# Kernel optimization log

Measured on AMD Instinct MI355X. Metric: run time of the kernel, lower is better.

The kernel has to match this reference:

```python
import jax, jax.numpy as jnp
import numpy as np
import math

B, S, D, H = 2, 2048, 1024, 16
DK = D // H

def setup_inputs() -> dict:
    key = jax.random.key(0)
    ks = jax.random.split(key, 12)
    s = 1.0 / math.sqrt(D)
    inp = {
        'input_q': jax.random.normal(ks[0], (B, S, D), jnp.float32),
        'input_k': jax.random.normal(ks[1], (B, S, D), jnp.float32),
        'input_v': jax.random.normal(ks[2], (B, S, D), jnp.float32),
        'mask': jax.random.randint(ks[3], (B, 1, S, S), 0, 2, jnp.int32),
        'Wq': jax.random.normal(ks[4], (D, D), jnp.float32) * s,
        'bq': jnp.zeros((D,), jnp.float32),
        'Wk': jax.random.normal(ks[5], (D, D), jnp.float32) * s,
        'bk': jnp.zeros((D,), jnp.float32),
        'Wv': jax.random.normal(ks[6], (D, D), jnp.float32) * s,
        'bv': jnp.zeros((D,), jnp.float32),
        'Wo': jax.random.normal(ks[7], (D, D), jnp.float32) * s,
        'bo': jnp.zeros((D,), jnp.float32),
    }
    return inp

def reference(input_q, input_k, input_v, mask, Wq, bq, Wk, bk, Wv, bv, Wo, bo):
    # Linear projections (torch Linear: x @ W.T + b), split into heads: [B,H,S,DK]
    q = (input_q @ Wq.T + bq).reshape(B, S, H, DK).transpose(0, 2, 1, 3)
    k = (input_k @ Wk.T + bk).reshape(B, S, H, DK).transpose(0, 2, 1, 3)
    v = (input_v @ Wv.T + bv).reshape(B, S, H, DK).transpose(0, 2, 1, 3)
    scores = jnp.einsum('bhqd,bhkd->bhqk', q, k) / math.sqrt(DK)
    scores = jnp.where(mask == 0, jnp.float32(-1e9), scores)
    attn = jax.nn.softmax(scores, axis=-1)
    out = jnp.einsum('bhqk,bhkd->bhqd', attn, v)
    out = out.transpose(0, 2, 1, 3).reshape(B, S, D)
    return out @ Wo.T + bo
```

## Files before the change

### kernel.cpp

```cpp
#include <hip/hip_runtime.h>
#include <math.h>

#define kB 2
#define kS 2048
#define kD 1024
#define kH 16
#define kM (kB * kS)

#define kC 0.180336880f

typedef unsigned short u16;
typedef unsigned int u32;
typedef unsigned long long u64;
typedef short s16x8 __attribute__((ext_vector_type(8)));
typedef float f32x4 __attribute__((ext_vector_type(4)));

__device__ __forceinline__ u16 f2bf(float f) {
    u32 u = __float_as_uint(f);
    u += 0x7FFFu + ((u >> 16) & 1u);
    return (u16)(u >> 16);
}

__device__ __forceinline__ u32 cvt_pk_bf16(float lo, float hi) {
    u32 r;
    asm("v_cvt_pk_bf16_f32 %0, %1, %2" : "=v"(r) : "v"(lo), "v"(hi));
    return r;
}

typedef __attribute__((address_space(1))) void as1_void;
typedef __attribute__((address_space(3))) void as3_void;
__device__ __forceinline__ void async_copy16(const void* g, void* l) {
    __builtin_amdgcn_global_load_lds((as1_void*)(unsigned long long)g,
                                     (as3_void*)(unsigned)(unsigned long long)l,
                                     16, 0, 0);
}

__global__ __launch_bounds__(256) void prep(
        const float* __restrict__ xq, const float* __restrict__ xk, const float* __restrict__ xv,
        const float* __restrict__ Wq, const float* __restrict__ Wk,
        const float* __restrict__ Wv, const float* __restrict__ Wo,
        const int* __restrict__ msk,
        u16* __restrict__ xqb, u16* __restrict__ xkb, u16* __restrict__ xvb,
        u16* __restrict__ wqb, u16* __restrict__ wkb, u16* __restrict__ wvb,
        u16* __restrict__ wob, u64* __restrict__ prepM) {
    const int bid = blockIdx.x;
    const int tid = threadIdx.x;
    if (bid < 16384) {
        const float* in;
        u16* out;
        int i;
        float sc = 1.0f;
        if (bid < 12288) {
            const int z = bid >> 12;
            in = z == 0 ? xq : (z == 1 ? xk : xv);
            out = z == 0 ? xqb : (z == 1 ? xkb : xvb);
            i = (bid & 4095) * 256 + tid;
        } else {
            const int z = (bid - 12288) >> 10;
            in = z == 0 ? Wq : (z == 1 ? Wk : (z == 2 ? Wv : Wo));
            out = z == 0 ? wqb : (z == 1 ? wkb : (z == 2 ? wvb : wob));
            if (z == 0) sc = kC;
            i = ((bid - 12288) & 1023) * 256 + tid;
        }
        const float4 v = ((const float4*)in)[i];
        ushort4 o;
        o.x = f2bf(v.x * sc); o.y = f2bf(v.y * sc);
        o.z = f2bf(v.z * sc); o.w = f2bf(v.w * sc);
        ((ushort4*)out)[i] = o;
    } else {
        const int wid = (bid - 16384) * 4 + (tid >> 6);
        const int lane = tid & 63;
        const int kt = wid & 31, qb = (wid >> 5) & 127, b = wid >> 12;
        const int q = qb * 16 + (lane & 15);
        const int kbase = kt * 64 + ((lane >> 4) << 2);
        const int* mrow = msk + ((size_t)b * kS + q) * kS;
        u64 keep = 0;
#pragma unroll
        for (int e = 0; e < 16; ++e) {
            const int k = kbase + (e >> 2) * 16 + (e & 3);
            const u64 bl = __ballot(mrow[k] != 0);
            if (lane == e) keep = bl;
        }
        if (lane < 16)
            prepM[(((size_t)b * 128 + qb) * 32 + kt) * 16 + lane] = keep;
    }
}

template <int MODE, int TILEM>
__device__ __forceinline__ void gemm_bt_body(const u16* __restrict__ A,
                                             const u16* __restrict__ W,
                                             const float* __restrict__ bias,
                                             void* __restrict__ Cp,
                                             const float bscale) {
    constexpr int FM = TILEM / 32;
    __shared__ u16 As[TILEM * 64];
    __shared__ u16 Bs[128 * 64];
    const int tid = threadIdx.x;
    const int wave = tid >> 6, lane = tid & 63;
    const int l15 = lane & 15, quad = lane >> 4, l7 = lane & 7;
    const int wr = wave >> 1, wc = wave & 1;
    const int m0 = (MODE == 3 ? blockIdx.x : blockIdx.y) * TILEM;
    const int n0 = (MODE == 3 ? blockIdx.y : blockIdx.x) * 128;

    const int srow = lane >> 3;
    const int schk = l7 ^ srow;
    const u16* gA = A + (size_t)(m0 + (TILEM / 4) * wave + srow) * kD + schk * 8;
    const u16* gB = W + (size_t)(n0 + 32 * wave + srow) * kD + schk * 8;
    u16* lA = As + ((TILEM / 4) * wave) * 64;
    u16* lB = Bs + (32 * wave) * 64;

    f32x4 acc[FM][4];
#pragma unroll
    for (int i = 0; i < FM; ++i)
#pragma unroll
        for (int j = 0; j < 4; ++j) acc[i][j] = (f32x4)0.f;

    for (int kt = 0; kt < kD; kt += 64) {
        __syncthreads();
#pragma unroll
        for (int i = 0; i < TILEM / 32; ++i)
            async_copy16(gA + (size_t)(8 * i) * kD + kt, lA + (8 * i) * 64);
#pragma unroll
        for (int i = 0; i < 4; ++i)
            async_copy16(gB + (size_t)(8 * i) * kD + kt, lB + (8 * i) * 64);
        __syncthreads();

#pragma unroll
        for (int s = 0; s < 2; ++s) {
            const int rdoff = ((s * 4 + quad) ^ l7) * 8;
            s16x8 af[FM], bf[4];
#pragma unroll
            for (int fm = 0; fm < FM; ++fm)
                af[fm] = *(const s16x8*)(As + (wr * (TILEM / 2) + fm * 16 + l15) * 64 + rdoff);
#pragma unroll
            for (int fn = 0; fn < 4; ++fn)
                bf[fn] = *(const s16x8*)(Bs + (wc * 64 + fn * 16 + l15) * 64 + rdoff);
#pragma unroll
            for (int fm = 0; fm < FM; ++fm)
#pragma unroll
                for (int fn = 0; fn < 4; ++fn)
                    acc[fm][fn] = __builtin_amdgcn_mfma_f32_16x16x32_bf16(
                        af[fm], bf[fn], acc[fm][fn], 0, 0, 0);
        }
    }

    if constexpr (MODE == 3) {
#pragma unroll
        for (int fn = 0; fn < 4; ++fn) {
            const int sglob = n0 + wc * 64 + fn * 16 + l15;
            const int bb = sglob >> 11, ss = sglob & (kS - 1);
#pragma unroll
            for (int fm = 0; fm < FM; ++fm) {
                const int dglob = m0 + wr * (TILEM / 2) + fm * 16 + quad * 4;
                const float4 b4 = *(const float4*)(bias + dglob);
                const float bb4[4] = {b4.x * bscale, b4.y * bscale,
                                      b4.z * bscale, b4.w * bscale};
                const int hh = dglob >> 6, dd = dglob & 63;
                u16* base = (u16*)Cp + ((size_t)(bb * kH + hh) * 64 + dd) * kS + ss;
#pragma unroll
                for (int r = 0; r < 4; ++r)
                    base[(size_t)r * kS] = f2bf(acc[fm][fn][r] + bb4[r]);
            }
        }
    } else {
#pragma unroll
        for (int fn = 0; fn < 4; ++fn) {
            const int col = n0 + wc * 64 + fn * 16 + l15;
            const float bv = bias[col] * bscale;
#pragma unroll
            for (int fm = 0; fm < FM; ++fm) {
                const int row = m0 + wr * (TILEM / 2) + fm * 16 + quad * 4;
#pragma unroll
                for (int r = 0; r < 4; ++r) {
                    const float v = acc[fm][fn][r] + bv;
                    if constexpr (MODE == 0)
                        ((u16*)Cp)[(size_t)(row + r) * kD + col] = f2bf(v);
                    else
                        ((float*)Cp)[(size_t)(row + r) * kD + col] = v;
                }
            }
        }
    }
}

__global__ __launch_bounds__(256) void qkv_gemm(
        const u16* __restrict__ xq, const u16* __restrict__ xk, const u16* __restrict__ xv,
        const u16* __restrict__ wq, const u16* __restrict__ wk, const u16* __restrict__ wv,
        const float* __restrict__ bq, const float* __restrict__ bk, const float* __restrict__ bv,
        u16* __restrict__ q, u16* __restrict__ k, u16* __restrict__ vt) {
    const int z = blockIdx.z;
    if (z == 0)      gemm_bt_body<0, 128>(xq, wq, bq, q, kC);
    else if (z == 1) gemm_bt_body<0, 128>(xk, wk, bk, k, 1.f);
    else             gemm_bt_body<3, 128>(wv, xv, bv, vt, 1.f);
}

__global__ __launch_bounds__(256) void o_gemm(const u16* __restrict__ A,
                                              const u16* __restrict__ W,
                                              const float* __restrict__ bias,
                                              float* __restrict__ C) {
    gemm_bt_body<2, 64>(A, W, bias, C, 1.f);
}

__global__ __launch_bounds__(256) void attn_mfma(const u16* __restrict__ Qb,
                                                 const u16* __restrict__ Kb,
                                                 const u16* __restrict__ Vt,
                                                 const u64* __restrict__ prepM,
                                                 u16* __restrict__ Ob) {
    __shared__ u16 Qs[64 * 64];
    __shared__ u16 Ks[64 * 64];
    __shared__ u16 Vs[64 * 64];
    __shared__ u16 Ps[64 * 64];

    const int tid = threadIdx.x;
    const int wave = tid >> 6, lane = tid & 63;
    const int l15 = lane & 15, quad = lane >> 4, l7 = lane & 7;
    const int q0 = blockIdx.x * 64;
    const int b = blockIdx.y >> 4, h = blockIdx.y & 15;

    const int srow = lane >> 3;
    const int schk = l7 ^ srow;

    {
        const u16* g0 = Qb + ((size_t)(b * kS + q0 + 16 * wave + srow)) * kD + h * 64 + schk * 8;
        async_copy16(g0, Qs + (16 * wave) * 64);
        async_copy16(g0 + 8 * kD, Qs + (16 * wave + 8) * 64);
    }
    const u16* gK0 = Kb + ((size_t)(b * kS + 16 * wave + srow)) * kD + h * 64 + schk * 8;
    const u16* gV0 = Vt + ((size_t)((b * kH + h) * 64 + 16 * wave + srow)) * kS + schk * 8;

    const int wave_u = __builtin_amdgcn_readfirstlane(wave);
    const u64* mbase = prepM + (((size_t)b * 128 + blockIdx.x * 4 + wave_u) * 32) * 16;

    s16x8 onesf;
#pragma unroll
    for (int i = 0; i < 8; ++i) onesf[i] = (short)0x3F80;

    f32x4 oacc[4];
#pragma unroll
    for (int i = 0; i < 4; ++i) oacc[i] = (f32x4)0.f;
    f32x4 lacc = (f32x4)0.f;

    __syncthreads();
    s16x8 bq[2];
    bq[0] = *(const s16x8*)(Qs + (16 * wave + l15) * 64 + ((0 + quad) ^ l7) * 8);
    bq[1] = *(const s16x8*)(Qs + (16 * wave + l15) * 64 + ((4 + quad) ^ l7) * 8);
    u16* psrow = Ps + (16 * wave + l15) * 64;

    for (int kt = 0; kt < kS; kt += 64) {
        __syncthreads();
        async_copy16(gK0 + (size_t)kt * kD, Ks + (16 * wave) * 64);
        async_copy16(gK0 + (size_t)(kt + 8) * kD, Ks + (16 * wave + 8) * 64);
        async_copy16(gV0 + kt, Vs + (16 * wave) * 64);
        async_copy16(gV0 + 8 * kS + kt, Vs + (16 * wave + 8) * 64);
        __syncthreads();

        f32x4 s[4];
#pragma unroll
        for (int fn = 0; fn < 4; ++fn) s[fn] = (f32x4)0.f;
#pragma unroll
        for (int kc = 0; kc < 2; ++kc)
#pragma unroll
            for (int fn = 0; fn < 4; ++fn) {
                const s16x8 ak = *(const s16x8*)(Ks + (fn * 16 + l15) * 64 + ((kc * 4 + quad) ^ l7) * 8);
                s[fn] = __builtin_amdgcn_mfma_f32_16x16x32_bf16(ak, bq[kc], s[fn], 0, 0, 0);
            }

        const u64* mt = mbase + (kt >> 6) * 16;
#pragma unroll
        for (int fn = 0; fn < 4; ++fn)
#pragma unroll
            for (int r = 0; r < 4; ++r) {
                const u64 mm = mt[fn * 4 + r];
                const float p = exp2f(s[fn][r]);
                float pm;
                asm("v_cndmask_b32 %0, 0, %1, %2" : "=v"(pm) : "v"(p), "s"(mm));
                s[fn][r] = pm;
            }

#pragma unroll
        for (int fn = 0; fn < 4; ++fn) {
            uint2 o;
            o.x = cvt_pk_bf16(s[fn][0], s[fn][1]);
            o.y = cvt_pk_bf16(s[fn][2], s[fn][3]);
            const int chunk = fn * 2 + (quad >> 1);
            *(uint2*)(psrow + ((chunk ^ l7) * 8) + (quad & 1) * 4) = o;
        }

#pragma unroll
        for (int kc = 0; kc < 2; ++kc) {
            const s16x8 bp = *(const s16x8*)(psrow + ((kc * 4 + quad) ^ l7) * 8);
            lacc = __builtin_amdgcn_mfma_f32_16x16x32_bf16(onesf, bp, lacc, 0, 0, 0);
#pragma unroll
            for (int fd = 0; fd < 4; ++fd) {
                const s16x8 av = *(const s16x8*)(Vs + (fd * 16 + l15) * 64 + ((kc * 4 + quad) ^ l7) * 8);
                oacc[fd] = __builtin_amdgcn_mfma_f32_16x16x32_bf16(av, bp, oacc[fd], 0, 0, 0);
            }
        }
    }

    const float inv = 1.f / lacc[0];
    const size_t orow = (size_t)(b * kS + q0 + 16 * wave + l15);
#pragma unroll
    for (int fd = 0; fd < 4; ++fd) {
        uint2 o;
        o.x = cvt_pk_bf16(oacc[fd][0] * inv, oacc[fd][1] * inv);
        o.y = cvt_pk_bf16(oacc[fd][2] * inv, oacc[fd][3] * inv);
        *(uint2*)(Ob + orow * kD + h * 64 + fd * 16 + quad * 4) = o;
    }
}

extern "C" void kernel_launch(void* const* d_in, const int* in_sizes, int n_in,
                              void* d_out, int out_size, void* d_ws, size_t ws_size,
                              hipStream_t stream) {
    const float* xq = (const float*)d_in[0];
    const float* xk = (const float*)d_in[1];
    const float* xv = (const float*)d_in[2];
    const int*  msk = (const int*)d_in[3];
    const float* Wq = (const float*)d_in[4];
    const float* bq = (const float*)d_in[5];
    const float* Wk = (const float*)d_in[6];
    const float* bk = (const float*)d_in[7];
    const float* Wv = (const float*)d_in[8];
    const float* bv = (const float*)d_in[9];
    const float* Wo = (const float*)d_in[10];
    const float* bo = (const float*)d_in[11];
    float* out = (float*)d_out;

    const size_t NX = (size_t)kM * kD;
    const size_t NW = (size_t)kD * kD;

    u64* prepM = (u64*)d_ws;
    u16* p = (u16*)((char*)d_ws + (1 << 20));
    u16* xqb = p; p += NX;
    u16* xkb = p; p += NX;
    u16* xvb = p; p += NX;
    u16* wqb = p; p += NW;
    u16* wkb = p; p += NW;
    u16* wvb = p; p += NW;
    u16* wob = p; p += NW;
    u16* qb  = p; p += NX;
    u16* kb  = p; p += NX;
    u16* vtb = p; p += NX;
    u16* ab  = xqb;

    prep<<<18432, 256, 0, stream>>>(xq, xk, xv, Wq, Wk, Wv, Wo, msk,
                                    xqb, xkb, xvb, wqb, wkb, wvb, wob, prepM);

    dim3 gq(kD / 128, kM / 128, 3);
    qkv_gemm<<<gq, 256, 0, stream>>>(xqb, xkb, xvb, wqb, wkb, wvb, bq, bk, bv, qb, kb, vtb);

    dim3 ga(kS / 64, kB * kH);
    attn_mfma<<<ga, 256, 0, stream>>>(qb, kb, vtb, prepM, ab);

    dim3 go(kD / 128, kM / 64);
    o_gemm<<<go, 256, 0, stream>>>(ab, wob, bo, out);
}
```

Measured before the change: 274.1 us.

## Double-buffer K/V tiles in attention with prefetch and MFMA priority hints

Restructures the attention loop so the next K/V tile is copied asynchronously into a second LDS buffer while the current tile is computed. This replaces the two barriers per iteration with one, and hides global load latency behind the MFMA work. It also preloads the mask words and V fragments into registers early, uses the hardware exp2 builtin, and raises wave priority around the MFMA sections. Q is staged in the P buffer to save LDS. The cost is higher LDS and register use, which may reduce occupancy.

```diff
diff --git a/kernel.cpp b/kernel.cpp
--- a/kernel.cpp
+++ b/kernel.cpp
@@ -14,6 +14,12 @@
 typedef unsigned long long u64;
 typedef short s16x8 __attribute__((ext_vector_type(8)));
 typedef float f32x4 __attribute__((ext_vector_type(4)));
+
+#if __has_builtin(__builtin_amdgcn_exp2f)
+#define EXP2(x) __builtin_amdgcn_exp2f(x)
+#else
+#define EXP2(x) exp2f(x)
+#endif
 
 __device__ __forceinline__ u16 f2bf(float f) {
     u32 u = __float_as_uint(f);
@@ -201,15 +207,86 @@
     gemm_bt_body<2, 64>(A, W, bias, C, 1.f);
 }
 
+__device__ __forceinline__ void attn_tile(
+        const int kt, u16* __restrict__ cur, u16* __restrict__ nxt, const bool do_stage,
+        const u16* __restrict__ gK0, const u16* __restrict__ gV0,
+        const u64* __restrict__ mbase,
+        const s16x8 bq0, const s16x8 bq1, const s16x8 onesf,
+        u16* __restrict__ psrow,
+        f32x4 oacc[4], f32x4& lacc,
+        const int l15, const int quad, const int l7, const int wave) {
+    if (do_stage) {
+        async_copy16(gK0 + (size_t)(kt + 64) * kD, nxt + (16 * wave) * 64);
+        async_copy16(gK0 + (size_t)(kt + 72) * kD, nxt + (16 * wave + 8) * 64);
+        async_copy16(gV0 + kt + 64, nxt + 4096 + (16 * wave) * 64);
+        async_copy16(gV0 + 8 * kS + kt + 64, nxt + 4096 + (16 * wave + 8) * 64);
+    }
+    const u64* mt = mbase + (kt >> 6) * 16;
+    u64 mk[16];
+#pragma unroll
+    for (int i = 0; i < 16; ++i) mk[i] = mt[i];
+
+    f32x4 s[4];
+#pragma unroll
+    for (int fn = 0; fn < 4; ++fn) s[fn] = (f32x4)0.f;
+    __builtin_amdgcn_s_setprio(1);
+#pragma unroll
+    for (int kc = 0; kc < 2; ++kc) {
+        const s16x8 bqf = kc ? bq1 : bq0;
+#pragma unroll
+        for (int fn = 0; fn < 4; ++fn) {
+            const s16x8 ak = *(const s16x8*)(cur + (fn * 16 + l15) * 64 + ((kc * 4 + quad) ^ l7) * 8);
+            s[fn] = __builtin_amdgcn_mfma_f32_16x16x32_bf16(ak, bqf, s[fn], 0, 0, 0);
+        }
+    }
+    __builtin_amdgcn_s_setprio(0);
+
+    s16x8 av[2][4];
+#pragma unroll
+    for (int kc = 0; kc < 2; ++kc)
+#pragma unroll
+        for (int fd = 0; fd < 4; ++fd)
+            av[kc][fd] = *(const s16x8*)(cur + 4096 + (fd * 16 + l15) * 64 + ((kc * 4 + quad) ^ l7) * 8);
+
+#pragma unroll
+    for (int fn = 0; fn < 4; ++fn)
+#pragma unroll
+        for (int r = 0; r < 4; ++r) {
+            const float p = EXP2(s[fn][r]);
+            float pm;
+            asm("v_cndmask_b32 %0, 0, %1, %2" : "=v"(pm) : "v"(p), "s"(mk[fn * 4 + r]));
+            s[fn][r] = pm;
+        }
+
+#pragma unroll
+    for (int fn = 0; fn < 4; ++fn) {
+        uint2 o;
+        o.x = cvt_pk_bf16(s[fn][0], s[fn][1]);
+        o.y = cvt_pk_bf16(s[fn][2], s[fn][3]);
+        const int chunk = fn * 2 + (quad >> 1);
+        *(uint2*)(psrow + ((chunk ^ l7) * 8) + (quad & 1) * 4) = o;
+    }
+
+    __builtin_amdgcn_s_setprio(1);
+#pragma unroll
+    for (int kc = 0; kc < 2; ++kc) {
+        const s16x8 bp = *(const s16x8*)(psrow + ((kc * 4 + quad) ^ l7) * 8);
+        lacc = __builtin_amdgcn_mfma_f32_16x16x32_bf16(onesf, bp, lacc, 0, 0, 0);
+#pragma unroll
+        for (int fd = 0; fd < 4; ++fd)
+            oacc[fd] = __builtin_amdgcn_mfma_f32_16x16x32_bf16(av[kc][fd], bp, oacc[fd], 0, 0, 0);
+    }
+    __builtin_amdgcn_s_setprio(0);
+    __syncthreads();
+}
+
 __global__ __launch_bounds__(256) void attn_mfma(const u16* __restrict__ Qb,
                                                  const u16* __restrict__ Kb,
                                                  const u16* __restrict__ Vt,
                                                  const u64* __restrict__ prepM,
                                                  u16* __restrict__ Ob) {
-    __shared__ u16 Qs[64 * 64];
-    __shared__ u16 Ks[64 * 64];
-    __shared__ u16 Vs[64 * 64];
-    __shared__ u16 Ps[64 * 64];
+    __shared__ u16 Bs2[2][8192];
+    __shared__ u16 Ps[4096];
 
     const int tid = threadIdx.x;
     const int wave = tid >> 6, lane = tid & 63;
@@ -222,11 +299,15 @@
 
     {
         const u16* g0 = Qb + ((size_t)(b * kS + q0 + 16 * wave + srow)) * kD + h * 64 + schk * 8;
-        async_copy16(g0, Qs + (16 * wave) * 64);
-        async_copy16(g0 + 8 * kD, Qs + (16 * wave + 8) * 64);
+        async_copy16(g0, Ps + (16 * wave) * 64);
+        async_copy16(g0 + 8 * kD, Ps + (16 * wave + 8) * 64);
     }
     const u16* gK0 = Kb + ((size_t)(b * kS + 16 * wave + srow)) * kD + h * 64 + schk * 8;
     const u16* gV0 = Vt + ((size_t)((b * kH + h) * 64 + 16 * wave + srow)) * kS + schk * 8;
+    async_copy16(gK0, Bs2[0] + (16 * wave) * 64);
+    async_copy16(gK0 + (size_t)8 * kD, Bs2[0] + (16 * wave + 8) * 64);
+    async_copy16(gV0, Bs2[0] + 4096 + (16 * wave) * 64);
+    async_copy16(gV0 + 8 * kS, Bs2[0] + 4096 + (16 * wave + 8) * 64);
 
     const int wave_u = __builtin_amdgcn_readfirstlane(wave);
     const u64* mbase = prepM + (((size_t)b * 128 + blockIdx.x * 4 + wave_u) * 32) * 16;
@@ -241,61 +322,18 @@
     f32x4 lacc = (f32x4)0.f;
 
     __syncthreads();
-    s16x8 bq[2];
-    bq[0] = *(const s16x8*)(Qs + (16 * wave + l15) * 64 + ((0 + quad) ^ l7) * 8);
-    bq[1] = *(const s16x8*)(Qs + (16 * wave + l15) * 64 + ((4 + quad) ^ l7) * 8);
+    s16x8 bq0, bq1;
+    bq0 = *(const s16x8*)(Ps + (16 * wave + l15) * 64 + ((0 + quad) ^ l7) * 8);
+    bq1 = *(const s16x8*)(Ps + (16 * wave + l15) * 64 + ((4 + quad) ^ l7) * 8);
     u16* psrow = Ps + (16 * wave + l15) * 64;
 
-    for (int kt = 0; kt < kS; kt += 64) {
-        __syncthreads();
-        async_copy16(gK0 + (size_t)kt * kD, Ks + (16 * wave) * 64);
-        async_copy16(gK0 + (size_t)(kt + 8) * kD, Ks + (16 * wave + 8) * 64);
-        async_copy16(gV0 + kt, Vs + (16 * wave) * 64);
-        async_copy16(gV0 + 8 * kS + kt, Vs + (16 * wave + 8) * 64);
-        __syncthreads();
-
-        f32x4 s[4];
-#pragma unroll
-        for (int fn = 0; fn < 4; ++fn) s[fn] = (f32x4)0.f;
-#pragma unroll
-        for (int kc = 0; kc < 2; ++kc)
-#pragma unroll
-            for (int fn = 0; fn < 4; ++fn) {
-                const s16x8 ak = *(const s16x8*)(Ks + (fn * 16 + l15) * 64 + ((kc * 4 + quad) ^ l7) * 8);
-                s[fn] = __builtin_amdgcn_mfma_f32_16x16x32_bf16(ak, bq[kc], s[fn], 0, 0, 0);
-            }
-
-        const u64* mt = mbase + (kt >> 6) * 16;
-#pragma unroll
-        for (int fn = 0; fn < 4; ++fn)
-#pragma unroll
-            for (int r = 0; r < 4; ++r) {
-                const u64 mm = mt[fn * 4 + r];
-                const float p = exp2f(s[fn][r]);
-                float pm;
-                asm("v_cndmask_b32 %0, 0, %1, %2" : "=v"(pm) : "v"(p), "s"(mm));
-                s[fn][r] = pm;
-            }
-
-#pragma unroll
-        for (int fn = 0; fn < 4; ++fn) {
-            uint2 o;
-            o.x = cvt_pk_bf16(s[fn][0], s[fn][1]);
-            o.y = cvt_pk_bf16(s[fn][2], s[fn][3]);
-            const int chunk = fn * 2 + (quad >> 1);
-            *(uint2*)(psrow + ((chunk ^ l7) * 8) + (quad & 1) * 4) = o;
-        }
-
-#pragma unroll
-        for (int kc = 0; kc < 2; ++kc) {
-            const s16x8 bp = *(const s16x8*)(psrow + ((kc * 4 + quad) ^ l7) * 8);
-            lacc = __builtin_amdgcn_mfma_f32_16x16x32_bf16(onesf, bp, lacc, 0, 0, 0);
-#pragma unroll
-            for (int fd = 0; fd < 4; ++fd) {
-                const s16x8 av = *(const s16x8*)(Vs + (fd * 16 + l15) * 64 + ((kc * 4 + quad) ^ l7) * 8);
-                oacc[fd] = __builtin_amdgcn_mfma_f32_16x16x32_bf16(av, bp, oacc[fd], 0, 0, 0);
-            }
-        }
+    for (int ti = 0; ti < 32; ti += 2) {
+        attn_tile(ti * 64, Bs2[0], Bs2[1], true,
+                  gK0, gV0, mbase, bq0, bq1, onesf, psrow, oacc, lacc,
+                  l15, quad, l7, wave);
+        attn_tile(ti * 64 + 64, Bs2[1], Bs2[0], ti + 2 < 32,
+                  gK0, gV0, mbase, bq0, bq1, onesf, psrow, oacc, lacc,
+                  l15, quad, l7, wave);
     }
 
     const float inv = 1.f / lacc[0];
```

Result: faster. 258.4 us (-5.7%).
